# Optimization experiments

Measured on AMD Instinct MI355X. Metric: run time of the kernel, lower is better.

## Reference

```python
import jax, jax.numpy as jnp
import numpy as np

EMBED_DIM = 768
NUM_HEADS = 12
HEAD_DIM = EMBED_DIM // NUM_HEADS
SCALE = HEAD_DIM ** -0.5


def setup_inputs() -> dict:
    key = jax.random.key(0)
    k_x, k_wqkv, k_bqkv, k_wfc, k_bfc = jax.random.split(key, 5)
    B, S, D = 32, 577, EMBED_DIM
    x = jax.random.normal(k_x, (B, S, D), dtype=jnp.float32)
    # torch Linear default init ~ U(-1/sqrt(fan_in), 1/sqrt(fan_in)); scale suffices
    lim = 1.0 / np.sqrt(D)
    w_qkv = jax.random.uniform(k_wqkv, (D, 3 * D), jnp.float32, -lim, lim)
    b_qkv = jax.random.uniform(k_bqkv, (3 * D,), jnp.float32, -lim, lim)
    w_fc = jax.random.uniform(k_wfc, (D, D), jnp.float32, -lim, lim)
    b_fc = jax.random.uniform(k_bfc, (D,), jnp.float32, -lim, lim)
    return {"x": x, "w_qkv": w_qkv, "b_qkv": b_qkv, "w_fc": w_fc, "b_fc": b_fc}


def reference(x, w_qkv, b_qkv, w_fc, b_fc):
    B, S, D = x.shape
    H, Dh = NUM_HEADS, HEAD_DIM
    qkv = x @ w_qkv + b_qkv                      # [B,S,3D]
    qkv = qkv.reshape(B, S, 3, H, Dh)
    q, k, v = jnp.moveaxis(qkv, 2, 0)            # each [B,S,H,Dh]
    # scores: [B,H,S,S]
    attn = jnp.einsum('bqhd,bkhd->bhqk', q, k) * SCALE
    attn = jax.nn.softmax(attn, axis=-1)
    out = jnp.einsum('bhqk,bkhd->bqhd', attn, v).reshape(B, S, D)
    # dropout in eval mode -> identity
    return out @ w_fc + b_fc
```

## Files before the change

### kernel.cpp

```cpp
#include <hip/hip_runtime.h>
#include <hip/hip_bf16.h>
#include <stdint.h>

typedef __attribute__((ext_vector_type(8))) short short8;
typedef __attribute__((ext_vector_type(4))) float f32x4;

typedef __attribute__((address_space(3))) uint8_t lds_u8;
typedef __attribute__((address_space(1))) uint8_t glb_u8;

__device__ __forceinline__ void load_lds_16(const void* g, void* l) {
    __builtin_amdgcn_global_load_lds((glb_u8*)g, (lds_u8*)l, 16, 0, 0);
}

__device__ __forceinline__ unsigned short f2b(float f) {
    __hip_bfloat16 h = __float2bfloat16(f);
    return __builtin_bit_cast(unsigned short, h);
}
__device__ __forceinline__ ushort2 f2b2(float a, float b) {
    __hip_bfloat162 h = __float22bfloat162_rn(float2{a, b});
    ushort2 r;
    __builtin_memcpy(&r, &h, sizeof(r));
    return r;
}
__device__ __forceinline__ float b2f(unsigned short u) {
    unsigned int x = ((unsigned int)u) << 16;
    return __builtin_bit_cast(float, x);
}

constexpr int Bz = 32, Ss = 577, Dd = 768, Hh = 12;
constexpr int Mm = Bz * Ss;
constexpr int QKV_N = 3 * Dd;
constexpr float SCALE_L2E = 0.125f * 1.4426950408889634f;

__global__ void prep_fused(const float* __restrict__ x, unsigned short* __restrict__ xb,
                           const float* __restrict__ w_qkv, unsigned short* __restrict__ wqkvT,
                           const float* __restrict__ w_fc, unsigned short* __restrict__ wfcT) {
    constexpr int N4 = Mm * Dd / 4;
    constexpr int NC = N4 / 256;
    constexpr int NT1 = (QKV_N / 32) * (Dd / 32);
    __shared__ unsigned short tile[32][33];

    const int bid = blockIdx.x;
    const int tid = threadIdx.x;
    if (bid < NC) {
        int i = bid * 256 + tid;
        float4 v = ((const float4*)x)[i];
        ushort4 o;
        o.x = f2b(v.x); o.y = f2b(v.y); o.z = f2b(v.z); o.w = f2b(v.w);
        ((ushort4*)xb)[i] = o;
        return;
    }
    const float* src; unsigned short* dst; int R, C, bx, by;
    if (bid < NC + NT1) {
        int b2 = bid - NC;
        src = w_qkv; dst = wqkvT; R = Dd; C = QKV_N;
        bx = b2 % (QKV_N / 32); by = b2 / (QKV_N / 32);
    } else {
        int b2 = bid - NC - NT1;
        src = w_fc; dst = wfcT; R = Dd; C = Dd;
        bx = b2 % (Dd / 32); by = b2 / (Dd / 32);
    }
    int c0 = bx * 32, r0 = by * 32;
    int tx = tid & 31, ty = tid >> 5;
#pragma unroll
    for (int i = 0; i < 4; ++i)
        tile[ty + i * 8][tx] = f2b(src[(size_t)(r0 + ty + i * 8) * C + c0 + tx]);
    __syncthreads();
#pragma unroll
    for (int i = 0; i < 4; ++i) {
        int rr = ty + i * 8;
        dst[(size_t)(c0 + rr) * R + r0 + tx] = tile[tx][rr];
    }
}

template <int N_, bool OUT_BF16>
__global__ __launch_bounds__(512, 2)
void gemm256(const unsigned short* __restrict__ A,
             const unsigned short* __restrict__ Bt,
             const float* __restrict__ bias,
             void* __restrict__ Cout) {
    constexpr int K = 768;
    constexpr int NX = N_ / 256;
    constexpr int NY = (Mm + 255) / 256;
    constexpr int NWG = NX * NY;
    constexpr int QC = NWG >> 3, RC = NWG & 7;
    extern __shared__ __align__(16) uint8_t smem[];

    const int tid = threadIdx.x;
    const int wave = tid >> 6, lane = tid & 63;
    const int quad = lane >> 4, lc = lane & 15;
    const int wm = wave >> 2, wn = wave & 3;

    const int orig = blockIdx.y * NX + blockIdx.x;
    const int xcd = orig & 7, lid = orig >> 3;
    const int wgid = (xcd < RC ? xcd * (QC + 1) : RC * (QC + 1) + (xcd - RC) * QC) + lid;
    const int tm = (wgid / NX) * 256;
    const int tn = (wgid % NX) * 256;

    const int lrw = wave * 8 + (lane >> 3);
    const unsigned short* apS[2];
    const unsigned short* bpS[2];
#pragma unroll
    for (int s = 0; s < 2; ++s) {
        const int lr = s * 64 + lrw;
        const int chun = (lane & 7) ^ (lr & 7);
        const int trow = lr * 2 + (chun >> 2);
        int ar = tm + trow; if (ar >= Mm) ar = Mm - 1;
        apS[s] = A + (size_t)ar * K + (chun & 3) * 8;
        const int br = tn + trow;
        bpS[s] = Bt + (size_t)br * K + (chun & 3) * 8;
    }

    auto stage = [&](int kb, int buf) {
        uint8_t* d = smem + buf * 32768 + wave * 1024;
        const int ko = kb * 32;
        load_lds_16(apS[0] + ko, d);
        load_lds_16(apS[1] + ko, d + 8192);
        load_lds_16(bpS[0] + ko, d + 16384);
        load_lds_16(bpS[1] + ko, d + 24576);
    };

    const int slotS = (((lane & 1) << 2) + quad) ^ ((lc >> 1) & 7);
    const int aoff = (wm * 64 + (lc >> 1)) * 128 + slotS * 16;
    const int boff = 16384 + (wn * 32 + (lc >> 1)) * 128 + slotS * 16;

    short8 af[8], bf[4];
    auto readfr = [&](int buf) {
        const uint8_t* p = smem + buf * 32768;
#pragma unroll
        for (int m = 0; m < 8; ++m) af[m] = *(const short8*)(p + aoff + m * 1024);
#pragma unroll
        for (int n = 0; n < 4; ++n) bf[n] = *(const short8*)(p + boff + n * 1024);
    };

    f32x4 acc[8][4] = {};
    auto mfmas = [&]() {
        __builtin_amdgcn_s_setprio(1);
#pragma unroll
        for (int m = 0; m < 8; ++m)
#pragma unroll
            for (int n = 0; n < 4; ++n)
                acc[m][n] = __builtin_amdgcn_mfma_f32_16x16x32_bf16(af[m], bf[n], acc[m][n], 0, 0, 0);
        __builtin_amdgcn_s_setprio(0);
    };

    stage(0, 0);
    stage(1, 1);
    asm volatile("s_waitcnt vmcnt(4)" ::: "memory");
    __builtin_amdgcn_s_barrier();

#pragma unroll 1
    for (int t3 = 0; t3 < 7; ++t3) {
        const int T = t3 * 3;
#pragma unroll
        for (int u = 0; u < 3; ++u) {
            const int sb = (u + 2) % 3;
            stage(T + u + 2, sb);
            readfr(u);
            mfmas();
            asm volatile("s_waitcnt vmcnt(4)" ::: "memory");
            __builtin_amdgcn_s_barrier();
        }
    }
    stage(23, 2);
    readfr(0);
    mfmas();
    asm volatile("s_waitcnt vmcnt(4)" ::: "memory");
    __builtin_amdgcn_s_barrier();
    readfr(1);
    mfmas();
    asm volatile("s_waitcnt vmcnt(0)" ::: "memory");
    __builtin_amdgcn_s_barrier();
    readfr(2);
    mfmas();
    __builtin_amdgcn_s_barrier();

    float bv[4];
#pragma unroll
    for (int j = 0; j < 4; ++j) bv[j] = bias[tn + wn * 64 + j * 16 + lc];

    float* ep = (float*)smem + wave * (16 * 68);
    const int erow = lane >> 2, ec = (lane & 3) * 16;
#pragma unroll
    for (int ia = 0; ia < 8; ++ia) {
#pragma unroll
        for (int j = 0; j < 4; ++j)
#pragma unroll
            for (int r = 0; r < 4; ++r)
                ep[(quad * 4 + r) * 68 + j * 16 + lc] = acc[ia][j][r] + bv[j];
        __threadfence_block();
        int grow = tm + wm * 128 + ia * 16 + erow;
        if (grow < Mm) {
            float4 c0 = *(float4*)&ep[erow * 68 + ec + 0];
            float4 c1 = *(float4*)&ep[erow * 68 + ec + 4];
            float4 c2 = *(float4*)&ep[erow * 68 + ec + 8];
            float4 c3 = *(float4*)&ep[erow * 68 + ec + 12];
            int gcol = tn + wn * 64 + ec;
            if constexpr (OUT_BF16) {
                unsigned short o[16];
                *(ushort2*)&o[0]  = f2b2(c0.x, c0.y);
                *(ushort2*)&o[2]  = f2b2(c0.z, c0.w);
                *(ushort2*)&o[4]  = f2b2(c1.x, c1.y);
                *(ushort2*)&o[6]  = f2b2(c1.z, c1.w);
                *(ushort2*)&o[8]  = f2b2(c2.x, c2.y);
                *(ushort2*)&o[10] = f2b2(c2.z, c2.w);
                *(ushort2*)&o[12] = f2b2(c3.x, c3.y);
                *(ushort2*)&o[14] = f2b2(c3.z, c3.w);
                unsigned short* op = (unsigned short*)Cout + (size_t)grow * N_ + gcol;
                *(short8*)(op + 0) = *(short8*)&o[0];
                *(short8*)(op + 8) = *(short8*)&o[8];
            } else {
                float* op = (float*)Cout + (size_t)grow * N_ + gcol;
                *(float4*)(op + 0)  = c0;
                *(float4*)(op + 4)  = c1;
                *(float4*)(op + 8)  = c2;
                *(float4*)(op + 12) = c3;
            }
        }
        __threadfence_block();
    }
}

__global__ __launch_bounds__(256)
void attn_kernel(const unsigned short* __restrict__ qkv,
                 unsigned short* __restrict__ outb) {
    __shared__ unsigned short Kt[2][64 * 64];
    __shared__ unsigned short Vt[2][80 * 72];
    __shared__ unsigned short Pq[4][32 * 72];

    const int tid = threadIdx.x;
    const int wave = tid >> 6, lane = tid & 63;
    const int quad = lane >> 4, lc = lane & 15;

    const int orig = (blockIdx.z * gridDim.y + blockIdx.y) * gridDim.x + blockIdx.x;
    const int wgid = (orig & 7) * 240 + (orig >> 3);
    const int qt = wgid % 5;
    const int h  = (wgid / 5) % Hh;
    const int b  = wgid / (5 * Hh);

    const unsigned short* qkvK = qkv + (size_t)b * Ss * QKV_N + h * 64 + 768;
    const unsigned short* qkvV = qkvK + 768;

    const int krow = lane >> 3;
    const int gch = (lane & 7) ^ krow;

    const int qbase = qt * 128 + wave * 32;
    short8 qf[2][2];
#pragma unroll
    for (int hf = 0; hf < 2; ++hf) {
        int qrow = qbase + hf * 16 + lc; if (qrow > Ss - 1) qrow = Ss - 1;
        const unsigned short* qp = qkv + (size_t)(b * Ss + qrow) * QKV_N + h * 64;
        qf[hf][0] = *(const short8*)(qp + quad * 8);
        qf[hf][1] = *(const short8*)(qp + 32 + quad * 8);
    }

    unsigned short* Pqw = Pq[wave];

    auto stage_K = [&](int tile, int buf) {
#pragma unroll
        for (int s = 0; s < 2; ++s) {
            int key = tile * 64 + s * 32 + wave * 8 + krow;
            load_lds_16(qkvK + (size_t)key * QKV_N + gch * 8,
                        (void*)&Kt[buf][(s * 32 + wave * 8) * 64]);
        }
    };
    auto load_V = [&](int tile, short8 v[2]) {
        int key = tile * 64 + lane;
#pragma unroll
        for (int s = 0; s < 2; ++s)
            v[s] = *(const short8*)(qkvV + (size_t)key * QKV_N + (s * 32 + wave * 8));
    };
    auto write_V = [&](short8 v[2], int buf) {
#pragma unroll
        for (int s = 0; s < 2; ++s)
#pragma unroll
            for (int j = 0; j < 8; ++j)
                Vt[buf][(s * 32 + wave * 8 + j) * 72 + lane] = (unsigned short)v[s][j];
    };

    if (tid < 72) {
        Vt[0][64 * 72 + tid] = 0x3F80;
        Vt[1][64 * 72 + tid] = 0x3F80;
    }

    f32x4 oacc[2][4] = {};
    f32x4 lacc[2] = {};

    auto tile_compute = [&](int buf) {
        const int sw = lc & 7;
        short8 k0[4], k1[4];
        #pragma unroll
        for (int f = 0; f < 4; ++f) {
            const unsigned short* kr = &Kt[buf][(f * 16 + lc) * 64];
            k0[f] = *(const short8*)(kr + (quad ^ sw) * 8);
            k1[f] = *(const short8*)(kr + ((quad ^ 4) ^ sw) * 8);
        }
        #pragma unroll
        for (int hf = 0; hf < 2; ++hf) {
            f32x4 sfr[4];
            __builtin_amdgcn_s_setprio(1);
            #pragma unroll
            for (int f = 0; f < 4; ++f) {
                f32x4 z = {};
                z = __builtin_amdgcn_mfma_f32_16x16x32_bf16(k0[f], qf[hf][0], z, 0, 0, 0);
                z = __builtin_amdgcn_mfma_f32_16x16x32_bf16(k1[f], qf[hf][1], z, 0, 0, 0);
                sfr[f] = z;
            }
            __builtin_amdgcn_s_setprio(0);
            #pragma unroll
            for (int f = 0; f < 4; ++f) {
                float p0 = __builtin_amdgcn_exp2f(sfr[f][0] * SCALE_L2E);
                float p1 = __builtin_amdgcn_exp2f(sfr[f][1] * SCALE_L2E);
                float p2 = __builtin_amdgcn_exp2f(sfr[f][2] * SCALE_L2E);
                float p3 = __builtin_amdgcn_exp2f(sfr[f][3] * SCALE_L2E);
                ushort2 lo = f2b2(p0, p1), hi = f2b2(p2, p3);
                ushort4 pk = {lo.x, lo.y, hi.x, hi.y};
                *(ushort4*)&Pqw[(hf * 16 + lc) * 72 + f * 16 + quad * 4] = pk;
            }
        }
        __threadfence_block();
        short8 pf[2][2];
        #pragma unroll
        for (int hf = 0; hf < 2; ++hf) {
            pf[hf][0] = *(const short8*)&Pqw[(hf * 16 + lc) * 72 + quad * 8];
            pf[hf][1] = *(const short8*)&Pqw[(hf * 16 + lc) * 72 + 32 + quad * 8];
        }
        __builtin_amdgcn_s_setprio(1);
        #pragma unroll
        for (int g = 0; g < 4; ++g) {
            short8 vf0 = *(const short8*)&Vt[buf][(g * 16 + lc) * 72 + quad * 8];
            short8 vf1 = *(const short8*)&Vt[buf][(g * 16 + lc) * 72 + 32 + quad * 8];
            oacc[0][g] = __builtin_amdgcn_mfma_f32_16x16x32_bf16(vf0, pf[0][0], oacc[0][g], 0, 0, 0);
            oacc[0][g] = __builtin_amdgcn_mfma_f32_16x16x32_bf16(vf1, pf[0][1], oacc[0][g], 0, 0, 0);
            oacc[1][g] = __builtin_amdgcn_mfma_f32_16x16x32_bf16(vf0, pf[1][0], oacc[1][g], 0, 0, 0);
            oacc[1][g] = __builtin_amdgcn_mfma_f32_16x16x32_bf16(vf1, pf[1][1], oacc[1][g], 0, 0, 0);
        }
        short8 vo0 = *(const short8*)&Vt[buf][(64 + lc) * 72 + quad * 8];
        short8 vo1 = *(const short8*)&Vt[buf][(64 + lc) * 72 + 32 + quad * 8];
        #pragma unroll
        for (int hf = 0; hf < 2; ++hf) {
            lacc[hf] = __builtin_amdgcn_mfma_f32_16x16x32_bf16(vo0, pf[hf][0], lacc[hf], 0, 0, 0);
            lacc[hf] = __builtin_amdgcn_mfma_f32_16x16x32_bf16(vo1, pf[hf][1], lacc[hf], 0, 0, 0);
        }
        __builtin_amdgcn_s_setprio(0);
    };

    short8 vreg[2];
    stage_K(0, 0);
    load_V(0, vreg);
    write_V(vreg, 0);
    __syncthreads();

    for (int kb = 0; kb < 8; ++kb) {
        const int buf = kb & 1;
        stage_K(kb + 1, buf ^ 1);
        load_V(kb + 1, vreg);
        tile_compute(buf);
        write_V(vreg, buf ^ 1);
        __syncthreads();
    }
    tile_compute(0);

    float ptl[2];
    {
        const unsigned short* k576 = qkvK + (size_t)576 * QKV_N;
        short8 kk0 = *(const short8*)(k576 + quad * 8);
        short8 kk1 = *(const short8*)(k576 + 32 + quad * 8);
        const unsigned short* v576 = qkvV + (size_t)576 * QKV_N;
#pragma unroll
        for (int hf = 0; hf < 2; ++hf) {
            float part = 0.f;
#pragma unroll
            for (int j = 0; j < 8; ++j)
                part += b2f((unsigned short)qf[hf][0][j]) * b2f((unsigned short)kk0[j])
                      + b2f((unsigned short)qf[hf][1][j]) * b2f((unsigned short)kk1[j]);
            part += __shfl_xor(part, 16, 64);
            part += __shfl_xor(part, 32, 64);
            ptl[hf] = __builtin_amdgcn_exp2f(part * SCALE_L2E);
#pragma unroll
            for (int g = 0; g < 4; ++g) {
                ushort4 vv = *(const ushort4*)(v576 + g * 16 + quad * 4);
                oacc[hf][g][0] += ptl[hf] * b2f(vv.x);
                oacc[hf][g][1] += ptl[hf] * b2f(vv.y);
                oacc[hf][g][2] += ptl[hf] * b2f(vv.z);
                oacc[hf][g][3] += ptl[hf] * b2f(vv.w);
            }
        }
    }

#pragma unroll
    for (int hf = 0; hf < 2; ++hf) {
        float lq = __shfl(lacc[hf][0], lc, 64) + ptl[hf];
        float inv = 1.f / lq;
#pragma unroll
        for (int g = 0; g < 4; ++g) {
            ushort2 lo = f2b2(oacc[hf][g][0] * inv, oacc[hf][g][1] * inv);
            ushort2 hi = f2b2(oacc[hf][g][2] * inv, oacc[hf][g][3] * inv);
            ushort4 ob = {lo.x, lo.y, hi.x, hi.y};
            *(ushort4*)&Pqw[(hf * 16 + lc) * 72 + g * 16 + quad * 4] = ob;
        }
    }
    __threadfence_block();
#pragma unroll
    for (int p = 0; p < 4; ++p) {
        int lr = p * 8 + (lane >> 3), ch = lane & 7;
        int q = qbase + lr;
        if (q <= Ss - 1) {
            short8 vv = *(const short8*)&Pqw[lr * 72 + ch * 8];
            *(short8*)(outb + (size_t)(b * Ss + q) * Dd + h * 64 + ch * 8) = vv;
        }
    }
}

extern "C" void kernel_launch(void* const* d_in, const int* in_sizes, int n_in,
                              void* d_out, int out_size, void* d_ws, size_t ws_size,
                              hipStream_t stream) {
    const float* x     = (const float*)d_in[0];
    const float* w_qkv = (const float*)d_in[1];
    const float* b_qkv = (const float*)d_in[2];
    const float* w_fc  = (const float*)d_in[3];
    const float* b_fc  = (const float*)d_in[4];

    uint8_t* ws = (uint8_t*)d_ws;
    unsigned short* xb    = (unsigned short*)(ws + 0);
    unsigned short* wqkvT = (unsigned short*)(ws + 28360704);
    unsigned short* wfcT  = (unsigned short*)(ws + 31899648);
    unsigned short* qkv   = (unsigned short*)(ws + 33079296);
    unsigned short* attn  = (unsigned short*)(ws + 118161408);

    static bool lds_init = false;
    if (!lds_init) {
        hipFuncSetAttribute((const void*)gemm256<QKV_N, true>,
                            hipFuncAttributeMaxDynamicSharedMemorySize, 98304);
        hipFuncSetAttribute((const void*)gemm256<Dd, false>,
                            hipFuncAttributeMaxDynamicSharedMemorySize, 98304);
        lds_init = true;
    }

    constexpr int PREP_GRID = (Mm * Dd / 4) / 256 + (QKV_N / 32) * (Dd / 32) + (Dd / 32) * (Dd / 32);
    prep_fused<<<PREP_GRID, 256, 0, stream>>>(x, xb, w_qkv, wqkvT, w_fc, wfcT);

    gemm256<QKV_N, true><<<dim3(QKV_N / 256, (Mm + 255) / 256), 512, 98304, stream>>>(xb, wqkvT, b_qkv, qkv);

    attn_kernel<<<dim3(5, Hh, Bz), 256, 0, stream>>>(qkv, attn);

    gemm256<Dd, false><<<dim3(Dd / 256, (Mm + 255) / 256), 512, 98304, stream>>>(attn, wfcT, b_fc, d_out);
}
```

Baseline: 307.4 us.

## Enlarge attention query tile to 256 rows with XOR-swizzled LDS layouts

Each wave of the attention kernel now handles 64 query rows instead of 32, and each block 256 instead of 128, so every staged K/V tile is reused across twice as many queries and the grid drops from 5 to 3 query tiles per head. V and P tiles move from padded stride-72 rows to XOR-swizzled stride-64 rows to avoid LDS bank conflicts. The row-sum now uses an all-ones register operand instead of an extra LDS ones row, so the normalisation no longer needs a shuffle. In exchange, register pressure roughly doubles for the accumulators under launch_bounds(256,2), and the last query tile does more padded work (768 rows covering 577).

```diff
diff --git a/kernel.cpp b/kernel.cpp
--- a/kernel.cpp
+++ b/kernel.cpp
@@ -221,22 +221,23 @@
     }
 }
 
-__global__ __launch_bounds__(256)
+__global__ __launch_bounds__(256, 2)
 void attn_kernel(const unsigned short* __restrict__ qkv,
                  unsigned short* __restrict__ outb) {
     __shared__ unsigned short Kt[2][64 * 64];
-    __shared__ unsigned short Vt[2][80 * 72];
-    __shared__ unsigned short Pq[4][32 * 72];
+    __shared__ unsigned short Vt[2][64 * 64];
+    __shared__ unsigned short Pq[4][64 * 64];
 
     const int tid = threadIdx.x;
     const int wave = tid >> 6, lane = tid & 63;
     const int quad = lane >> 4, lc = lane & 15;
+    const int lsw = lc & 7;
 
     const int orig = (blockIdx.z * gridDim.y + blockIdx.y) * gridDim.x + blockIdx.x;
-    const int wgid = (orig & 7) * 240 + (orig >> 3);
-    const int qt = wgid % 5;
-    const int h  = (wgid / 5) % Hh;
-    const int b  = wgid / (5 * Hh);
+    const int wgid = (orig & 7) * 144 + (orig >> 3);
+    const int qt = wgid % 3;
+    const int h  = (wgid / 3) % Hh;
+    const int b  = wgid / (3 * Hh);
 
     const unsigned short* qkvK = qkv + (size_t)b * Ss * QKV_N + h * 64 + 768;
     const unsigned short* qkvV = qkvK + 768;
@@ -244,10 +245,10 @@
     const int krow = lane >> 3;
     const int gch = (lane & 7) ^ krow;
 
-    const int qbase = qt * 128 + wave * 32;
-    short8 qf[2][2];
-#pragma unroll
-    for (int hf = 0; hf < 2; ++hf) {
+    const int qbase = qt * 256 + wave * 64;
+    short8 qf[4][2];
+#pragma unroll
+    for (int hf = 0; hf < 4; ++hf) {
         int qrow = qbase + hf * 16 + lc; if (qrow > Ss - 1) qrow = Ss - 1;
         const unsigned short* qp = qkv + (size_t)(b * Ss + qrow) * QKV_N + h * 64;
         qf[hf][0] = *(const short8*)(qp + quad * 8);
@@ -256,6 +257,10 @@
 
     unsigned short* Pqw = Pq[wave];
 
+    short8 ones;
+#pragma unroll
+    for (int j = 0; j < 8; ++j) ones[j] = (short)0x3F80;
+
     auto stage_K = [&](int tile, int buf) {
 #pragma unroll
         for (int s = 0; s < 2; ++s) {
@@ -274,32 +279,29 @@
 #pragma unroll
         for (int s = 0; s < 2; ++s)
 #pragma unroll
-            for (int j = 0; j < 8; ++j)
-                Vt[buf][(s * 32 + wave * 8 + j) * 72 + lane] = (unsigned short)v[s][j];
-    };
-
-    if (tid < 72) {
-        Vt[0][64 * 72 + tid] = 0x3F80;
-        Vt[1][64 * 72 + tid] = 0x3F80;
-    }
-
-    f32x4 oacc[2][4] = {};
-    f32x4 lacc[2] = {};
+            for (int j = 0; j < 8; ++j) {
+                int d = s * 32 + wave * 8 + j;
+                Vt[buf][d * 64 + ((((lane >> 3) ^ (d & 7)) << 3) | (lane & 7))] =
+                    (unsigned short)v[s][j];
+            }
+    };
+
+    f32x4 oacc[4][4] = {};
+    f32x4 lacc[4] = {};
 
     auto tile_compute = [&](int buf) {
-        const int sw = lc & 7;
         short8 k0[4], k1[4];
-        #pragma unroll
+#pragma unroll
         for (int f = 0; f < 4; ++f) {
             const unsigned short* kr = &Kt[buf][(f * 16 + lc) * 64];
-            k0[f] = *(const short8*)(kr + (quad ^ sw) * 8);
-            k1[f] = *(const short8*)(kr + ((quad ^ 4) ^ sw) * 8);
-        }
-        #pragma unroll
-        for (int hf = 0; hf < 2; ++hf) {
+            k0[f] = *(const short8*)(kr + ((quad ^ lsw) << 3));
+            k1[f] = *(const short8*)(kr + (((quad ^ 4) ^ lsw) << 3));
+        }
+#pragma unroll
+        for (int hf = 0; hf < 4; ++hf) {
             f32x4 sfr[4];
             __builtin_amdgcn_s_setprio(1);
-            #pragma unroll
+#pragma unroll
             for (int f = 0; f < 4; ++f) {
                 f32x4 z = {};
                 z = __builtin_amdgcn_mfma_f32_16x16x32_bf16(k0[f], qf[hf][0], z, 0, 0, 0);
@@ -307,7 +309,8 @@
                 sfr[f] = z;
             }
             __builtin_amdgcn_s_setprio(0);
-            #pragma unroll
+            const int qrow64 = (hf * 16 + lc) * 64;
+#pragma unroll
             for (int f = 0; f < 4; ++f) {
                 float p0 = __builtin_amdgcn_exp2f(sfr[f][0] * SCALE_L2E);
                 float p1 = __builtin_amdgcn_exp2f(sfr[f][1] * SCALE_L2E);
@@ -315,32 +318,34 @@
                 float p3 = __builtin_amdgcn_exp2f(sfr[f][3] * SCALE_L2E);
                 ushort2 lo = f2b2(p0, p1), hi = f2b2(p2, p3);
                 ushort4 pk = {lo.x, lo.y, hi.x, hi.y};
-                *(ushort4*)&Pqw[(hf * 16 + lc) * 72 + f * 16 + quad * 4] = pk;
+                *(ushort4*)&Pqw[qrow64 + ((((2 * f + (quad >> 1)) ^ lsw) << 3) | ((quad & 1) << 2))] = pk;
             }
         }
         __threadfence_block();
-        short8 pf[2][2];
-        #pragma unroll
-        for (int hf = 0; hf < 2; ++hf) {
-            pf[hf][0] = *(const short8*)&Pqw[(hf * 16 + lc) * 72 + quad * 8];
-            pf[hf][1] = *(const short8*)&Pqw[(hf * 16 + lc) * 72 + 32 + quad * 8];
+
+        short8 pf[4][2];
+#pragma unroll
+        for (int hf = 0; hf < 4; ++hf) {
+            const int qrow64 = (hf * 16 + lc) * 64;
+            pf[hf][0] = *(const short8*)&Pqw[qrow64 + ((quad ^ lsw) << 3)];
+            pf[hf][1] = *(const short8*)&Pqw[qrow64 + (((quad ^ 4) ^ lsw) << 3)];
         }
         __builtin_amdgcn_s_setprio(1);
-        #pragma unroll
+#pragma unroll
         for (int g = 0; g < 4; ++g) {
-            short8 vf0 = *(const short8*)&Vt[buf][(g * 16 + lc) * 72 + quad * 8];
-            short8 vf1 = *(const short8*)&Vt[buf][(g * 16 + lc) * 72 + 32 + quad * 8];
-            oacc[0][g] = __builtin_amdgcn_mfma_f32_16x16x32_bf16(vf0, pf[0][0], oacc[0][g], 0, 0, 0);
-            oacc[0][g] = __builtin_amdgcn_mfma_f32_16x16x32_bf16(vf1, pf[0][1], oacc[0][g], 0, 0, 0);
-            oacc[1][g] = __builtin_amdgcn_mfma_f32_16x16x32_bf16(vf0, pf[1][0], oacc[1][g], 0, 0, 0);
-            oacc[1][g] = __builtin_amdgcn_mfma_f32_16x16x32_bf16(vf1, pf[1][1], oacc[1][g], 0, 0, 0);
-        }
-        short8 vo0 = *(const short8*)&Vt[buf][(64 + lc) * 72 + quad * 8];
-        short8 vo1 = *(const short8*)&Vt[buf][(64 + lc) * 72 + 32 + quad * 8];
-        #pragma unroll
-        for (int hf = 0; hf < 2; ++hf) {
-            lacc[hf] = __builtin_amdgcn_mfma_f32_16x16x32_bf16(vo0, pf[hf][0], lacc[hf], 0, 0, 0);
-            lacc[hf] = __builtin_amdgcn_mfma_f32_16x16x32_bf16(vo1, pf[hf][1], lacc[hf], 0, 0, 0);
+            const unsigned short* vr = &Vt[buf][(g * 16 + lc) * 64];
+            short8 vf0 = *(const short8*)(vr + ((quad ^ lsw) << 3));
+            short8 vf1 = *(const short8*)(vr + (((quad ^ 4) ^ lsw) << 3));
+#pragma unroll
+            for (int hf = 0; hf < 4; ++hf) {
+                oacc[hf][g] = __builtin_amdgcn_mfma_f32_16x16x32_bf16(vf0, pf[hf][0], oacc[hf][g], 0, 0, 0);
+                oacc[hf][g] = __builtin_amdgcn_mfma_f32_16x16x32_bf16(vf1, pf[hf][1], oacc[hf][g], 0, 0, 0);
+            }
+        }
+#pragma unroll
+        for (int hf = 0; hf < 4; ++hf) {
+            lacc[hf] = __builtin_amdgcn_mfma_f32_16x16x32_bf16(ones, pf[hf][0], lacc[hf], 0, 0, 0);
+            lacc[hf] = __builtin_amdgcn_mfma_f32_16x16x32_bf16(ones, pf[hf][1], lacc[hf], 0, 0, 0);
         }
         __builtin_amdgcn_s_setprio(0);
     };
@@ -361,14 +366,14 @@
     }
     tile_compute(0);
 
-    float ptl[2];
+    float ptl[4];
     {
         const unsigned short* k576 = qkvK + (size_t)576 * QKV_N;
         short8 kk0 = *(const short8*)(k576 + quad * 8);
         short8 kk1 = *(const short8*)(k576 + 32 + quad * 8);
         const unsigned short* v576 = qkvV + (size_t)576 * QKV_N;
 #pragma unroll
-        for (int hf = 0; hf < 2; ++hf) {
+        for (int hf = 0; hf < 4; ++hf) {
             float part = 0.f;
 #pragma unroll
             for (int j = 0; j < 8; ++j)
@@ -389,24 +394,24 @@
     }
 
 #pragma unroll
-    for (int hf = 0; hf < 2; ++hf) {
-        float lq = __shfl(lacc[hf][0], lc, 64) + ptl[hf];
-        float inv = 1.f / lq;
+    for (int hf = 0; hf < 4; ++hf) {
+        float inv = 1.f / (lacc[hf][0] + ptl[hf]);
+        const int qrow64 = (hf * 16 + lc) * 64;
 #pragma unroll
         for (int g = 0; g < 4; ++g) {
             ushort2 lo = f2b2(oacc[hf][g][0] * inv, oacc[hf][g][1] * inv);
             ushort2 hi = f2b2(oacc[hf][g][2] * inv, oacc[hf][g][3] * inv);
             ushort4 ob = {lo.x, lo.y, hi.x, hi.y};
-            *(ushort4*)&Pqw[(hf * 16 + lc) * 72 + g * 16 + quad * 4] = ob;
+            *(ushort4*)&Pqw[qrow64 + ((((2 * g + (quad >> 1)) ^ lsw) << 3) | ((quad & 1) << 2))] = ob;
         }
     }
     __threadfence_block();
 #pragma unroll
-    for (int p = 0; p < 4; ++p) {
+    for (int p = 0; p < 8; ++p) {
         int lr = p * 8 + (lane >> 3), ch = lane & 7;
         int q = qbase + lr;
         if (q <= Ss - 1) {
-            short8 vv = *(const short8*)&Pqw[lr * 72 + ch * 8];
+            short8 vv = *(const short8*)&Pqw[lr * 64 + ((ch ^ (lr & 7)) << 3)];
             *(short8*)(outb + (size_t)(b * Ss + q) * Dd + h * 64 + ch * 8) = vv;
         }
     }
@@ -442,7 +447,7 @@
 
     gemm256<QKV_N, true><<<dim3(QKV_N / 256, (Mm + 255) / 256), 512, 98304, stream>>>(xb, wqkvT, b_qkv, qkv);
 
-    attn_kernel<<<dim3(5, Hh, Bz), 256, 0, stream>>>(qkv, attn);
+    attn_kernel<<<dim3(3, Hh, Bz), 256, 0, stream>>>(qkv, attn);
 
     gemm256<Dd, false><<<dim3(Dd / 256, (Mm + 255) / 256), 512, 98304, stream>>>(attn, wfcT, b_fc, d_out);
 }
```

New measurement: 318.8 us. +3.7%, slower.
